# Optimization experiments

Measured on AMD Instinct MI355X. Metric: run time of the kernel, lower is better.

Reference implementation:

```python
import jax, jax.numpy as jnp
import numpy as np

B, N, M, C = 8, 2048, 2048, 512


def setup_inputs() -> dict:
    key = jax.random.key(0)
    ks = jax.random.split(key, 10)
    s = 1.0 / np.sqrt(C)
    dec_embed = jax.random.normal(ks[0], (B, N, C), dtype=jnp.float32)
    enc_embed = jax.random.normal(ks[1], (B, M, C), dtype=jnp.float32)
    trans_mat = (jax.random.uniform(ks[2], (B, N, M)) < 0.5).astype(jnp.float32)
    Wv = jax.random.uniform(ks[3], (C, C), minval=-s, maxval=s, dtype=jnp.float32)
    bv = jax.random.uniform(ks[4], (C,), minval=-s, maxval=s, dtype=jnp.float32)
    W1 = jax.random.uniform(ks[5], (C, C), minval=-s, maxval=s, dtype=jnp.float32)
    b1 = jax.random.uniform(ks[6], (C,), minval=-s, maxval=s, dtype=jnp.float32)
    W2 = jax.random.uniform(ks[7], (C, C), minval=-s, maxval=s, dtype=jnp.float32)
    b2 = jax.random.uniform(ks[8], (C,), minval=-s, maxval=s, dtype=jnp.float32)
    return {"dec_embed": dec_embed, "enc_embed": enc_embed, "trans_mat": trans_mat,
            "Wv": Wv, "bv": bv, "W1": W1, "b1": b1, "W2": W2, "b2": b2}


def reference(dec_embed, enc_embed, trans_mat, Wv, bv, W1, b1, W2, b2):
    # scores [B,N,M], elementwise-masked by trans_mat
    attn = jnp.einsum('bnc,bmc->bnm', dec_embed, enc_embed) * trans_mat
    # NONSTANDARD masked softmax: zeros participate in softmax (exp(0)=1 in denom),
    # then positions where attn==0 are re-zeroed.
    sm = jax.nn.softmax(attn, axis=-1)
    attn = jnp.where(attn != 0, sm, jnp.zeros((), attn.dtype))
    v = enc_embed @ Wv + bv                      # [B,M,C]
    v = jnp.tanh(jnp.einsum('bnm,bmc->bnc', attn, v))  # [B,N,C]
    g = dec_embed * v + dec_embed                # tanh-gate + residual
    h = jax.nn.relu(g @ W1 + b1)                 # Mlp fc1 + ReLU (drop=0)
    return h @ W2 + b2                           # Mlp fc2
```

## Files before the change

kernel.cpp:

```cpp
#include <hip/hip_runtime.h>
#include <math.h>

#define Bb 8
#define Nn 2048
#define Mm 2048
#define Cc 512

typedef __attribute__((ext_vector_type(8))) _Float16 hfrag;
typedef __attribute__((ext_vector_type(4))) float f4;
typedef __attribute__((ext_vector_type(4))) _Float16 h4;

__device__ __forceinline__ void gld16(const void* g, void* l) {
    __builtin_amdgcn_global_load_lds(
        (const __attribute__((address_space(1))) void*)g,
        (__attribute__((address_space(3))) void*)l, 16, 0, 0);
}

template<int EPI, int BN, int SWZ>
__global__ __launch_bounds__(256) void gemm_mfma(
    const _Float16* __restrict__ Ah, long sA, int lda,
    const _Float16* __restrict__ Bh, long sB, int ldb,
    const float* __restrict__ aux, long sAux, int ldaux,
    const _Float16* __restrict__ aux2,
    float* __restrict__ mlal,
    void* __restrict__ Cout, long sC, int ldc, int K, int GX)
{
    constexpr int NI  = (BN == 128) ? 4 : 2;
    constexpr int ASL = 512;
    constexpr int BSL = BN * 4;
    constexpr int NQ  = (ASL + BSL) / 256;

    __shared__ _Float16 As[2][128 * 32];
    __shared__ _Float16 Bs[2][BN * 32];

    int bx, by, bz;
    if (SWZ == 1) {
        const int id = blockIdx.x;
        bz = id & 7; bx = (id >> 3) % GX; by = (id >> 3) / GX;
    } else if (SWZ == 2) {
        const int id = blockIdx.x;
        bz = 0; bx = (id >> 3) % GX; by = (id & 7) + 8 * ((id >> 3) / GX);
    } else {
        bx = blockIdx.x; by = blockIdx.y; bz = 0;
    }

    const _Float16* A0 = Ah + (size_t)bz * sA;
    const _Float16* B0 = Bh + (size_t)bz * sB;

    const int tid  = threadIdx.x;
    const int wv   = tid >> 6;
    const int ln   = tid & 63;
    const int wx   = (BN == 128) ? (wv & 1) : 0;
    const int wy   = (BN == 128) ? (wv >> 1) : wv;
    const int lcol = ln & 15, quad = ln >> 4;
    const int row0w = wy * (NI * 16);
    const int col0w = wx * 64;

    const int rowBase = by * 128;
    const int colBase = bx * BN;

    const int soff = (quad ^ ((lcol >> 1) & 3)) * 8;

    f4 acc[NI][4];
    const f4 z4 = {0.f, 0.f, 0.f, 0.f};
    #pragma unroll
    for (int i = 0; i < NI; ++i)
        #pragma unroll
        for (int j = 0; j < 4; ++j) acc[i][j] = z4;

    const float* alb = (EPI == 2) ? (mlal + (size_t)bz * (2048 * 32)) : nullptr;
    _Float16 als[4] = {(_Float16)0.f, (_Float16)0.f, (_Float16)0.f, (_Float16)0.f};

    auto STAGE = [&](int k0, int p) {
        #pragma unroll
        for (int q = 0; q < NQ; ++q) {
            const int c = q * 256 + wv * 64 + ln;
            if (c < ASL) {
                const int r = c >> 2;
                const int g = (c & 3) ^ ((c >> 3) & 3);
                gld16(A0 + (size_t)(rowBase + r) * lda + k0 + g * 8, &As[p][c * 8]);
            } else {
                const int cb = c - ASL;
                const int r  = cb >> 2;
                const int g  = (cb & 3) ^ ((cb >> 3) & 3);
                gld16(B0 + (size_t)(colBase + r) * ldb + k0 + g * 8, &Bs[p][cb * 8]);
            }
        }
    };

    const int NT = K >> 5;
    STAGE(0, 0);
    __syncthreads();

    for (int t = 0; t < NT; ++t) {
        const int p = t & 1;
        if (t + 1 < NT) STAGE((t + 1) * 32, p ^ 1);

        if (EPI == 2 && (t & 1) == 0) {
            const int tt = t >> 1;
            #pragma unroll
            for (int j = 0; j < 4; ++j) {
                const int n = colBase + col0w + j * 16 + lcol;
                als[j] = (_Float16)alb[(size_t)n * 32 + tt];
            }
        }

        hfrag af[NI], bf_[4];
        #pragma unroll
        for (int i = 0; i < NI; ++i)
            af[i]  = *(const hfrag*)&As[p][(row0w + i * 16 + lcol) * 32 + soff];
        #pragma unroll
        for (int j = 0; j < 4; ++j)
            bf_[j] = *(const hfrag*)&Bs[p][(col0w + j * 16 + lcol) * 32 + soff];

        if (EPI == 2) {
            #pragma unroll
            for (int j = 0; j < 4; ++j) bf_[j] = bf_[j] * als[j];
        }

        #pragma unroll
        for (int i = 0; i < NI; ++i)
            #pragma unroll
            for (int j = 0; j < 4; ++j)
                acc[i][j] = __builtin_amdgcn_mfma_f32_16x16x32_f16(af[i], bf_[j], acc[i][j], 0, 0, 0);

        if (t + 1 < NT) __syncthreads();
    }

    const int crow0 = rowBase + row0w + quad * 4;
    const int ccol0 = colBase + col0w + lcol;

    if (EPI == 0) {
        _Float16* E = (_Float16*)Cout + (size_t)bz * sC;
        const float* Mk = aux + (size_t)bz * sAux;
        const int t = (rowBase + row0w) >> 6;

        f4 mk[NI];
        #pragma unroll
        for (int i = 0; i < NI; ++i)
            mk[i] = *(const f4*)(Mk + (size_t)ccol0 * ldaux + crow0 + i * 16);

        #pragma unroll
        for (int j = 0; j < 4; ++j) {
            const int n = ccol0 + j * 16;
            f4 mkn[NI];
            if (j < 3) {
                #pragma unroll
                for (int i = 0; i < NI; ++i)
                    mkn[i] = *(const f4*)(Mk + (size_t)(n + 16) * ldaux + crow0 + i * 16);
            }
            #pragma unroll
            for (int i = 0; i < NI; ++i)
                #pragma unroll
                for (int r = 0; r < 4; ++r) acc[i][j][r] *= mk[i][r];

            float mx = acc[0][j][0];
            #pragma unroll
            for (int i = 0; i < NI; ++i)
                #pragma unroll
                for (int r = 0; r < 4; ++r) mx = fmaxf(mx, acc[i][j][r]);
            mx = fmaxf(mx, __shfl_xor(mx, 16, 64));
            mx = fmaxf(mx, __shfl_xor(mx, 32, 64));
            float l0 = 0.f;
            #pragma unroll
            for (int i = 0; i < NI; ++i) {
                h4 ev;
                #pragma unroll
                for (int r = 0; r < 4; ++r) {
                    const float s = acc[i][j][r];
                    const float e = __expf(s - mx);
                    l0 += e;
                    ev[r] = (s == 0.f) ? (_Float16)0.f : (_Float16)e;
                }
                *(h4*)(E + (size_t)n * ldc + crow0 + i * 16) = ev;
            }
            l0 += __shfl_xor(l0, 16, 64);
            l0 += __shfl_xor(l0, 32, 64);
            if (quad == 0) {
                float2 p; p.x = mx; p.y = l0;
                ((float2*)mlal)[((size_t)bz * 2048 + n) * 32 + t] = p;
            }
            if (j < 3) {
                #pragma unroll
                for (int i = 0; i < NI; ++i) mk[i] = mkn[i];
            }
        }
    } else if (EPI == 1) {
        _Float16* C = (_Float16*)Cout;
        #pragma unroll
        for (int j = 0; j < 4; ++j) {
            const int col = ccol0 + j * 16;
            const float bi = aux[col];
            #pragma unroll
            for (int i = 0; i < NI; ++i) {
                const int rowb = crow0 + i * 16;
                const int bb = rowb >> 11, ml = rowb & 2047;
                h4 st;
                #pragma unroll
                for (int r = 0; r < 4; ++r) st[r] = (_Float16)(acc[i][j][r] + bi);
                *(h4*)(C + (size_t)bb * ((size_t)Cc * Mm) + (size_t)col * Mm + ml) = st;
            }
        }
    } else if (EPI == 2) {
        _Float16* C = (_Float16*)Cout + (size_t)bz * sC;
        const _Float16* Dg = aux2 + (size_t)bz * sC;
        #pragma unroll
        for (int i = 0; i < NI; ++i) {
            const int c0 = crow0 + i * 16;
            #pragma unroll
            for (int j = 0; j < 4; ++j) {
                const int n = ccol0 + j * 16;
                const h4 dv = *(const h4*)(Dg + (size_t)n * ldc + c0);
                h4 gv;
                #pragma unroll
                for (int r = 0; r < 4; ++r) {
                    const float a = acc[i][j][r];
                    const float th = 1.f - 2.f / (__expf(2.f * a) + 1.f);
                    gv[r] = (_Float16)((float)dv[r] * (1.f + th));
                }
                *(h4*)(C + (size_t)n * ldc + c0) = gv;
            }
        }
    } else if (EPI == 3) {
        _Float16* C = (_Float16*)Cout;
        #pragma unroll
        for (int i = 0; i < NI; ++i) {
            const int c0 = crow0 + i * 16;
            const f4 bi = *(const f4*)(aux + c0);
            #pragma unroll
            for (int j = 0; j < 4; ++j) {
                const int n = ccol0 + j * 16;
                h4 hv;
                #pragma unroll
                for (int r = 0; r < 4; ++r)
                    hv[r] = (_Float16)fmaxf(acc[i][j][r] + bi[r], 0.f);
                *(h4*)(C + (size_t)n * ldc + c0) = hv;
            }
        }
    } else {
        float* C = (float*)Cout;
        #pragma unroll
        for (int i = 0; i < NI; ++i) {
            const int c0 = crow0 + i * 16;
            const f4 bi = *(const f4*)(aux + c0);
            #pragma unroll
            for (int j = 0; j < 4; ++j) {
                const int n = ccol0 + j * 16;
                f4 ov;
                #pragma unroll
                for (int r = 0; r < 4; ++r) ov[r] = acc[i][j][r] + bi[r];
                *(f4*)(C + (size_t)n * ldc + c0) = ov;
            }
        }
    }
}

__global__ __launch_bounds__(64) void combine_kernel(
    const float* __restrict__ mlq, float* __restrict__ alpha)
{
    const int row = blockIdx.x * 64 + threadIdx.x;
    const float2* ml = (const float2*)mlq + (size_t)row * 32;
    float mt[32], lt[32];
    float m = -1e30f;
    #pragma unroll
    for (int t = 0; t < 32; ++t) {
        float2 p = ml[t];
        mt[t] = p.x; lt[t] = p.y;
        m = fmaxf(m, p.x);
    }
    float et[32], l = 0.f;
    #pragma unroll
    for (int t = 0; t < 32; ++t) {
        et[t] = __expf(mt[t] - m);
        l += lt[t] * et[t];
    }
    const float inv = 1.f / l;
    float* ap = alpha + (size_t)row * 32;
    #pragma unroll
    for (int t = 0; t < 32; ++t) ap[t] = et[t] * inv;
}

__global__ __launch_bounds__(256) void sconv(const float* __restrict__ x,
                                             _Float16* __restrict__ o)
{
    const size_t i = (size_t)blockIdx.x * 256 + threadIdx.x;
    f4 v = ((const f4*)x)[i];
    h4 hh;
    #pragma unroll
    for (int k = 0; k < 4; ++k) hh[k] = (_Float16)v[k];
    ((h4*)o)[i] = hh;
}

__global__ __launch_bounds__(256) void wconv(const float* s0, const float* s1, const float* s2,
                                             _Float16* d0, _Float16* d1, _Float16* d2)
{
    const float* Sm = blockIdx.z == 0 ? s0 : blockIdx.z == 1 ? s1 : s2;
    _Float16* D = blockIdx.z == 0 ? d0 : blockIdx.z == 1 ? d1 : d2;
    __shared__ float t[32][33];
    const int x = threadIdx.x & 31, y = threadIdx.x >> 5;
    const int gx = blockIdx.x * 32, gy = blockIdx.y * 32;
    #pragma unroll
    for (int yy = y; yy < 32; yy += 8)
        t[yy][x] = Sm[(size_t)(gy + yy) * 512 + gx + x];
    __syncthreads();
    #pragma unroll
    for (int yy = y; yy < 32; yy += 8)
        D[(size_t)(gx + yy) * 512 + gy + x] = (_Float16)t[x][yy];
}

extern "C" void kernel_launch(void* const* d_in, const int* in_sizes, int n_in,
                              void* d_out, int out_size, void* d_ws, size_t ws_size,
                              hipStream_t stream)
{
    const float* dec   = (const float*)d_in[0];
    const float* enc   = (const float*)d_in[1];
    const float* trans = (const float*)d_in[2];
    const float* Wv = (const float*)d_in[3];
    const float* bv = (const float*)d_in[4];
    const float* W1 = (const float*)d_in[5];
    const float* b1 = (const float*)d_in[6];
    const float* W2 = (const float*)d_in[7];
    const float* b2 = (const float*)d_in[8];

    char* ws = (char*)d_ws;
    _Float16* e     = (_Float16*)ws;
    float*    mlq   = (float*)(ws + 0x4000000);
    float*    alpha = (float*)(ws + 0x4400000);
    _Float16* dec_h = (_Float16*)(ws + 0x4600000);
    _Float16* Wvt   = (_Float16*)(ws + 0x5600000);
    _Float16* W1t   = Wvt + 262144;
    _Float16* W2t   = Wvt + 524288;
    _Float16* vT    = (_Float16*)(ws + 0x5800000);
    _Float16* g     = (_Float16*)(ws + 0x6800000);
    _Float16* h     = (_Float16*)(ws + 0x7800000);
    _Float16* enc_h = (_Float16*)d_out;

    sconv<<<dim3(8192), 256, 0, stream>>>(dec, dec_h);
    sconv<<<dim3(8192), 256, 0, stream>>>(enc, enc_h);
    wconv<<<dim3(16, 16, 3), 256, 0, stream>>>(Wv, W1, W2, Wvt, W1t, W2t);

    gemm_mfma<0, 128, 1><<<dim3(2048), 256, 0, stream>>>(
        enc_h, (long)Mm * Cc, 512,
        dec_h, (long)Nn * Cc, 512,
        trans, (long)Nn * Mm, 2048, nullptr, mlq,
        e, (long)Nn * Mm, 2048, 512, 16);

    combine_kernel<<<dim3(256), 64, 0, stream>>>(mlq, alpha);

    gemm_mfma<1, 64, 2><<<dim3(1024), 256, 0, stream>>>(
        enc_h, 0, 512, Wvt, 0, 512, bv, 0, 0, nullptr, nullptr,
        vT, 0, 0, 512, 8);

    gemm_mfma<2, 128, 1><<<dim3(512), 256, 0, stream>>>(
        vT, (long)Cc * Mm, 2048,
        e, (long)Nn * Mm, 2048,
        nullptr, 0, 512, dec_h, alpha,
        g, (long)Nn * Cc, 512, 2048, 16);

    gemm_mfma<3, 64, 0><<<dim3(256, 4), 256, 0, stream>>>(
        W1t, 0, 512, g, 0, 512, b1, 0, 0, nullptr, nullptr,
        h, 0, 512, 512, 0);

    gemm_mfma<4, 64, 0><<<dim3(256, 4), 256, 0, stream>>>(
        W2t, 0, 512, h, 0, 512, b2, 0, 0, nullptr, nullptr,
        d_out, 0, 512, 512, 0);
}
```

Measured before the change: 451.5 us.

## Triple-buffer GEMM LDS tiles with vmcnt waits and stage alpha scales in LDS

Moves the MFMA GEMM main loop from double to triple buffering. Tiles are prefetched two K-steps ahead, and explicit `s_waitcnt vmcnt` plus a raw `s_barrier` replace the full `__syncthreads`, so global-to-LDS loads overlap more compute. For the EPI==2 path, the per-column alpha scale factors are preloaded into an LDS table once, instead of being fetched from global memory every other iteration. The EPI==0 softmax epilogue now prefetches mask rows two columns ahead. The cost is about 56KB of LDS per block, which can lower occupancy, and more reliance on hand-tuned wait counts.

```diff
diff --git a/kernel.cpp b/kernel.cpp
--- a/kernel.cpp
+++ b/kernel.cpp
@@ -14,6 +14,13 @@
     __builtin_amdgcn_global_load_lds(
         (const __attribute__((address_space(1))) void*)g,
         (__attribute__((address_space(3))) void*)l, 16, 0, 0);
+}
+
+template<int N> __device__ __forceinline__ void wait_vmcnt() {
+    if constexpr (N == 0)      asm volatile("s_waitcnt vmcnt(0)" ::: "memory");
+    else if constexpr (N == 3) asm volatile("s_waitcnt vmcnt(3)" ::: "memory");
+    else if constexpr (N == 4) asm volatile("s_waitcnt vmcnt(4)" ::: "memory");
+    __builtin_amdgcn_sched_barrier(0);
 }
 
 template<int EPI, int BN, int SWZ>
@@ -30,8 +37,9 @@
     constexpr int BSL = BN * 4;
     constexpr int NQ  = (ASL + BSL) / 256;
 
-    __shared__ _Float16 As[2][128 * 32];
-    __shared__ _Float16 Bs[2][BN * 32];
+    __shared__ _Float16 As[3][128 * 32];
+    __shared__ _Float16 Bs[3][BN * 32];
+    __shared__ _Float16 AlS[(EPI == 2) ? 32 * 128 : 4];
 
     int bx, by, bz;
     if (SWZ == 1) {
@@ -68,7 +76,17 @@
         #pragma unroll
         for (int j = 0; j < 4; ++j) acc[i][j] = z4;
 
-    const float* alb = (EPI == 2) ? (mlal + (size_t)bz * (2048 * 32)) : nullptr;
+    if (EPI == 2) {
+        const float* alb = mlal + (size_t)bz * (2048 * 32);
+        #pragma unroll
+        for (int q = 0; q < 16; ++q) {
+            const int idx = q * 256 + tid;
+            const int col = idx >> 5, tt = idx & 31;
+            AlS[tt * 128 + col] = (_Float16)alb[(size_t)(colBase + col) * 32 + tt];
+        }
+        asm volatile("s_waitcnt lgkmcnt(0)" ::: "memory");
+        __builtin_amdgcn_sched_barrier(0);
+    }
     _Float16 als[4] = {(_Float16)0.f, (_Float16)0.f, (_Float16)0.f, (_Float16)0.f};
 
     auto STAGE = [&](int k0, int p) {
@@ -90,19 +108,19 @@
 
     const int NT = K >> 5;
     STAGE(0, 0);
-    __syncthreads();
-
+    STAGE(32, 1);
+    wait_vmcnt<NQ>();
+    __builtin_amdgcn_s_barrier();
+
+    int p = 0, pn2 = 2;
     for (int t = 0; t < NT; ++t) {
-        const int p = t & 1;
-        if (t + 1 < NT) STAGE((t + 1) * 32, p ^ 1);
+        if (t + 2 < NT) STAGE((t + 2) * 32, pn2);
 
         if (EPI == 2 && (t & 1) == 0) {
             const int tt = t >> 1;
             #pragma unroll
-            for (int j = 0; j < 4; ++j) {
-                const int n = colBase + col0w + j * 16 + lcol;
-                als[j] = (_Float16)alb[(size_t)n * 32 + tt];
-            }
+            for (int j = 0; j < 4; ++j)
+                als[j] = AlS[tt * 128 + col0w + j * 16 + lcol];
         }
 
         hfrag af[NI], bf_[4];
@@ -124,7 +142,13 @@
             for (int j = 0; j < 4; ++j)
                 acc[i][j] = __builtin_amdgcn_mfma_f32_16x16x32_f16(af[i], bf_[j], acc[i][j], 0, 0, 0);
 
-        if (t + 1 < NT) __syncthreads();
+        if (t + 1 < NT) {
+            if (t + 2 < NT) wait_vmcnt<NQ>();
+            else            wait_vmcnt<0>();
+            __builtin_amdgcn_s_barrier();
+        }
+        p   = (p   == 2) ? 0 : p + 1;
+        pn2 = (pn2 == 2) ? 0 : pn2 + 1;
     }
 
     const int crow0 = rowBase + row0w + quad * 4;
@@ -135,24 +159,27 @@
         const float* Mk = aux + (size_t)bz * sAux;
         const int t = (rowBase + row0w) >> 6;
 
-        f4 mk[NI];
+        f4 mkA[NI], mkB[NI];
         #pragma unroll
         for (int i = 0; i < NI; ++i)
-            mk[i] = *(const f4*)(Mk + (size_t)ccol0 * ldaux + crow0 + i * 16);
+            mkA[i] = *(const f4*)(Mk + (size_t)ccol0 * ldaux + crow0 + i * 16);
+        #pragma unroll
+        for (int i = 0; i < NI; ++i)
+            mkB[i] = *(const f4*)(Mk + (size_t)(ccol0 + 16) * ldaux + crow0 + i * 16);
 
         #pragma unroll
         for (int j = 0; j < 4; ++j) {
             const int n = ccol0 + j * 16;
-            f4 mkn[NI];
-            if (j < 3) {
+            f4 mkN[NI];
+            if (j < 2) {
                 #pragma unroll
                 for (int i = 0; i < NI; ++i)
-                    mkn[i] = *(const f4*)(Mk + (size_t)(n + 16) * ldaux + crow0 + i * 16);
+                    mkN[i] = *(const f4*)(Mk + (size_t)(n + 32) * ldaux + crow0 + i * 16);
             }
             #pragma unroll
             for (int i = 0; i < NI; ++i)
                 #pragma unroll
-                for (int r = 0; r < 4; ++r) acc[i][j][r] *= mk[i][r];
+                for (int r = 0; r < 4; ++r) acc[i][j][r] *= mkA[i][r];
 
             float mx = acc[0][j][0];
             #pragma unroll
@@ -177,12 +204,14 @@
             l0 += __shfl_xor(l0, 16, 64);
             l0 += __shfl_xor(l0, 32, 64);
             if (quad == 0) {
-                float2 p; p.x = mx; p.y = l0;
-                ((float2*)mlal)[((size_t)bz * 2048 + n) * 32 + t] = p;
-            }
-            if (j < 3) {
-                #pragma unroll
-                for (int i = 0; i < NI; ++i) mk[i] = mkn[i];
+                float2 pq; pq.x = mx; pq.y = l0;
+                ((float2*)mlal)[((size_t)bz * 2048 + n) * 32 + t] = pq;
+            }
+            #pragma unroll
+            for (int i = 0; i < NI; ++i) { mkA[i] = mkB[i]; }
+            if (j < 2) {
+                #pragma unroll
+                for (int i = 0; i < NI; ++i) mkB[i] = mkN[i];
             }
         }
     } else if (EPI == 1) {
```

After: 444.8 us. No clear change (-1.5%).
